# Kernel optimization log

Measured on AMD Instinct MI355X. Metric: run time of the kernel, lower is better.

Reference implementation:

```python
import jax, jax.numpy as jnp
import numpy as np

DEPTH = 3


def _gather_nei(feats, graph):
    # feats: [B, M, F], graph: [B, N, NB] -> [B, N, NB, F]
    return jax.vmap(lambda f, g: f[g])(feats, graph)


def setup_inputs() -> dict:
    B, N, NB, NBOND = 64, 120, 10, 250
    AF, BF, H = 82, 6, 300
    key = jax.random.key(0)
    ks = jax.random.split(key, 14)
    inp = {
        "atom_feats_1": jax.random.normal(ks[0], (B, N, AF), dtype=jnp.float32),
        "bond_feats": jax.random.normal(ks[1], (B, NBOND, BF), dtype=jnp.float32),
        "atom_graph": jax.random.randint(ks[2], (B, N, NB), 0, N, dtype=jnp.int64),
        "bond_graph": jax.random.randint(ks[3], (B, N, NB), 0, NBOND, dtype=jnp.int64),
        "num_nbs": jax.random.randint(ks[4], (B, N), 0, NB, dtype=jnp.int64),
        "n_atoms": jax.random.randint(ks[5], (B,), 1, N, dtype=jnp.int64),
        "mask_neis": jax.random.randint(ks[6], (B, N, NB, 1), 0, 2) > 0,
        "mask_atoms": jax.random.randint(ks[7], (B, N, 1), 0, 2) > 0,
        # parameters (Linear weights stored as [in, out]); dropout is eval-mode (identity)
        "W_fc1": jax.random.normal(ks[8], (AF, H), dtype=jnp.float32) * 0.05,
        "W_gc_nei": jax.random.normal(ks[9], (H + BF, H), dtype=jnp.float32) * 0.05,
        "b_gc_nei": jnp.zeros((H,), dtype=jnp.float32),
        "W_gc_atom": jax.random.normal(ks[10], (2 * H, H), dtype=jnp.float32) * 0.05,
        "b_gc_atom": jnp.zeros((H,), dtype=jnp.float32),
        "W_fc2a": jax.random.normal(ks[11], (H, H), dtype=jnp.float32) * 0.05,
        "W_fc2b": jax.random.normal(ks[12], (BF, H), dtype=jnp.float32) * 0.05,
        "W_fc2": jax.random.normal(ks[13], (H, H), dtype=jnp.float32) * 0.05,
    }
    return inp


def reference(atom_feats_1, bond_feats, atom_graph, bond_graph, num_nbs, n_atoms,
              mask_neis, mask_atoms, W_fc1, W_gc_nei, b_gc_nei, W_gc_atom,
              b_gc_atom, W_fc2a, W_fc2b, W_fc2):
    zero = jnp.float32(0)
    atom_feats = jax.nn.relu(atom_feats_1 @ W_fc1)                 # [B,N,H]
    bondnei_feats = _gather_nei(bond_feats, bond_graph)            # [B,N,NB,BF]
    local_feats = None
    for i in range(DEPTH):
        atomnei_feats = _gather_nei(atom_feats, atom_graph)        # [B,N,NB,H]
        if i + 1 == DEPTH:
            an = atomnei_feats @ W_fc2a                            # [B,N,NB,H]
            bn = bondnei_feats @ W_fc2b                            # [B,N,NB,H]
            nei = jnp.where(mask_neis, an * bn, zero).sum(-2)      # [B,N,H]
            self_feats = atom_feats @ W_fc2                        # [B,N,H]
            local_feats = jnp.where(mask_atoms, self_feats * nei, zero)
        else:
            cat = jnp.concatenate([atomnei_feats, bondnei_feats], axis=-1)
            nei = jax.nn.relu(cat @ W_gc_nei + b_gc_nei)           # [B,N,NB,H]
            nei = jnp.where(mask_neis, nei, zero).sum(-2)          # [B,N,H]
            update = jnp.concatenate([atom_feats, nei], axis=-1)   # [B,N,2H]
            atom_feats = jax.nn.relu(update @ W_gc_atom + b_gc_atom)
    return local_feats
```

## Files before the change

kernel.cpp:

```cpp
#include <hip/hip_runtime.h>
#include <hip/hip_bf16.h>

#define BATCH 64
#define NATOM 120
#define NNB 10
#define NBOND 250
#define AFDIM 82
#define BFDIM 6
#define HREAL 300
#define HP 320
#define NCT32 10
#define MA (BATCH*NATOM)
#define MB (BATCH*NBOND)

typedef short short8 __attribute__((ext_vector_type(8)));
typedef float f32x16 __attribute__((ext_vector_type(16)));
typedef unsigned int u32;
typedef u32 u32x2 __attribute__((ext_vector_type(2)));
typedef unsigned short u16;

__device__ __forceinline__ float bflo(u32 v) { return __builtin_bit_cast(float, v << 16); }
__device__ __forceinline__ float bfhi(u32 v) { return __builtin_bit_cast(float, v & 0xffff0000u); }
__device__ __forceinline__ u16 f2bf(float f) {
    __hip_bfloat16 h = __float2bfloat16(f);
    return __builtin_bit_cast(u16, h);
}

struct PackJob { const float* W; short8* dst; int Kreal, KT, KTfull, ktOff, blk0; };
struct Prep {
    const float* a1src; __hip_bfloat16* a1dst;
    const float* bsrc;  __hip_bfloat16* bdst;
    const int *mn, *agp, *bgp; u32* pk;
    PackJob j[8];
};

#define CONV1_BLKS 2880
#define CONV2_BLKS 2000
#define PACK_BASE  (CONV1_BLKS + CONV2_BLKS)
#define PACK_BLKS  275
#define PK_BASE    (PACK_BASE + PACK_BLKS)
#define PK_BLKS    300
#define PREP_BLKS  (PK_BASE + PK_BLKS)

__global__ __launch_bounds__(256) void prep_all(Prep cfg) {
    const int bid = blockIdx.x;
    const int tid = threadIdx.x;
    if (bid < CONV1_BLKS) {
        int id = bid * 256 + tid;
        int r = id / 96, c = id - r * 96;
        float f = (c < AFDIM) ? cfg.a1src[(size_t)r * AFDIM + c] : 0.f;
        cfg.a1dst[id] = __float2bfloat16(f);
    } else if (bid < PACK_BASE) {
        int id = (bid - CONV1_BLKS) * 256 + tid;
        int r = id >> 5, c = id & 31;
        float f = (c < BFDIM) ? cfg.bsrc[(size_t)r * BFDIM + c] : 0.f;
        cfg.bdst[id] = __float2bfloat16(f);
    } else if (bid < PK_BASE) {
        const int pid = bid - PACK_BASE;
        int ji = 0;
#pragma unroll
        for (int i = 1; i < 8; ++i) if (pid >= cfg.j[i].blk0) ji = i;
        const PackJob J = cfg.j[ji];
        int id = (pid - J.blk0) * 256 + tid;
        int n = NCT32 * J.KT * 64;
        if (id >= n) return;
        int lane = id & 63;
        int kt = (id >> 6) % J.KT;
        int ct = id / (J.KT * 64);
        int col = ct * 32 + (lane & 31);
        int kbase = kt * 16 + (lane >> 5) * 8;
        short8 v;
#pragma unroll
        for (int jj = 0; jj < 8; ++jj) {
            int k = kbase + jj;
            float f = (k < J.Kreal && col < HREAL) ? J.W[(size_t)k * HREAL + col] : 0.f;
            v[jj] = (short)f2bf(f);
        }
        J.dst[(size_t)(ct * J.KTfull + J.ktOff + kt) * 64 + lane] = v;
    } else {
        int id = (bid - PK_BASE) * 256 + tid;
        u32 w = 0;
        if (cfg.mn[id]) w = 0x80000000u | ((u32)cfg.agp[id] << 16) | (u32)cfg.bgp[id];
        cfg.pk[id] = w;
    }
}

template<int KT, int KT1, int WAVES, bool RELU, bool OUT1F, bool ADDF>
__device__ __forceinline__ void gemm_dev(
    int bx, int by, int tid,
    const __hip_bfloat16* __restrict__ A1,
    const __hip_bfloat16* __restrict__ A2,
    const short8* __restrict__ Wp,
    const float* __restrict__ bias0,
    const float* __restrict__ bias1,
    __hip_bfloat16* __restrict__ out0,
    __hip_bfloat16* __restrict__ out1,
    float* __restrict__ out1f,
    const float* __restrict__ addp) {
    const int lane = tid & 63;
    const int wv   = tid >> 6;
    const int m0   = bx * (32 * WAVES) + wv * 32;
    const int ct0  = by * 2;
    const int r1   = m0 + (lane & 31);
    const int koff = (lane >> 5) * 8;

    constexpr int S1  = KT1 * 16;
    constexpr int S2  = (KT - KT1) * 16;
    constexpr int CH  = (KT >= 10) ? 10 : KT;
    constexpr int NCH = KT / CH;

    f32x16 acc[2];
#pragma unroll
    for (int r = 0; r < 16; ++r) { acc[0][r] = 0.f; acc[1][r] = 0.f; }

    const short8* w0 = Wp + ((size_t)ct0 * KT) * 64 + lane;
    const short8* w1 = w0 + (size_t)KT * 64;

#pragma unroll
    for (int ch = 0; ch < NCH; ++ch) {
        short8 a[CH];
#pragma unroll
        for (int kt = 0; kt < CH; ++kt) {
            const int g = ch * CH + kt;
            if (g < KT1)
                a[kt] = *reinterpret_cast<const short8*>(A1 + (size_t)r1 * S1 + g * 16 + koff);
            else
                a[kt] = *reinterpret_cast<const short8*>(A2 + (size_t)r1 * S2 + (g - KT1) * 16 + koff);
        }
#pragma unroll
        for (int kt = 0; kt < CH; ++kt) {
            const int g = ch * CH + kt;
            acc[0] = __builtin_amdgcn_mfma_f32_32x32x16_bf16(a[kt], w0[(size_t)g * 64], acc[0], 0, 0, 0);
            acc[1] = __builtin_amdgcn_mfma_f32_32x32x16_bf16(a[kt], w1[(size_t)g * 64], acc[1], 0, 0, 0);
        }
    }

#pragma unroll
    for (int c = 0; c < 2; ++c) {
        const int ct = ct0 + c;
        const bool second = (ct >= NCT32);
        const int colb = second ? ct * 32 - HP : ct * 32;
        const int col = colb + (lane & 31);
        __hip_bfloat16* op = second ? out1 : out0;
        const float* bp = second ? bias1 : bias0;
        const float bb = (bp && col < HREAL) ? bp[col] : 0.f;
#pragma unroll
        for (int r = 0; r < 16; ++r) {
            const int row = m0 + (r & 3) + 8 * (r >> 2) + 4 * (lane >> 5);
            float v = acc[c][r] + bb;
            if (ADDF) v += addp[(size_t)row * HP + col];
            if (RELU) v = fmaxf(v, 0.f);
            if (second) {
                if (OUT1F) out1f[(size_t)row * HP + col] = v;
                else       out1[(size_t)row * HP + col] = __float2bfloat16(v);
            } else {
                op[(size_t)row * HP + col] = __float2bfloat16(v);
            }
        }
    }
}

#define FC1_BLKS  (MA/64 * 5)
#define BOND_BLKS (MB/64 * 10)
__global__ __launch_bounds__(128)
void k_input_gemms(const __hip_bfloat16* __restrict__ A1b,
                   const __hip_bfloat16* __restrict__ bondb,
                   const short8* __restrict__ pW1,
                   const short8* __restrict__ pWbd,
                   const float* __restrict__ bgn,
                   __hip_bfloat16* __restrict__ af0,
                   __hip_bfloat16* __restrict__ bondgc,
                   __hip_bfloat16* __restrict__ bnb) {
    const int bid = blockIdx.x;
    if (bid < FC1_BLKS) {
        gemm_dev<6, 6, 2, true, false, false>(bid % (MA/64), bid / (MA/64), threadIdx.x,
                                              A1b, A1b, pW1, nullptr, nullptr, af0, nullptr, nullptr, nullptr);
    } else {
        const int b2 = bid - FC1_BLKS;
        gemm_dev<2, 2, 2, false, false, false>(b2 % (MB/64), b2 / (MB/64), threadIdx.x,
                                               bondb, bondb, pWbd, bgn, nullptr, bondgc, bnb, nullptr, nullptr);
    }
}

__global__ __launch_bounds__(256)
void k_gemm_nu(const __hip_bfloat16* __restrict__ af, const short8* __restrict__ W,
               const float* __restrict__ bias1,
               __hip_bfloat16* __restrict__ Tb, float* __restrict__ U) {
    gemm_dev<20, 20, 4, false, true, false>(blockIdx.x, blockIdx.y, threadIdx.x,
                                            af, af, W, nullptr, bias1, Tb, nullptr, U, nullptr);
}

__global__ __launch_bounds__(128)
void k_gemm_bot(const __hip_bfloat16* __restrict__ neib, const short8* __restrict__ W,
                const float* __restrict__ U, __hip_bfloat16* __restrict__ afn) {
    gemm_dev<20, 20, 2, true, false, true>(blockIdx.x, blockIdx.y, threadIdx.x,
                                           neib, neib, W, nullptr, nullptr, afn, nullptr, nullptr, U);
}

__global__ __launch_bounds__(256)
void k_gemm_final(const __hip_bfloat16* __restrict__ af, const short8* __restrict__ W,
                  __hip_bfloat16* __restrict__ selfF, __hip_bfloat16* __restrict__ A2f) {
    gemm_dev<20, 20, 4, false, false, false>(blockIdx.x, blockIdx.y, threadIdx.x,
                                             af, af, W, nullptr, nullptr, selfF, A2f, nullptr, nullptr);
}

__global__ __launch_bounds__(320)
void gather2(const u32* __restrict__ T,
             const u32* __restrict__ BG,
             const u32* __restrict__ pk,
             u32* __restrict__ nei) {
    const int bn = blockIdx.x * 4 + threadIdx.x / 80;
    const int t2 = (threadIdx.x % 80) * 2;
    const int b  = bn / NATOM;
    const int base = bn * NNB;
    float lo0 = 0.f, hi0 = 0.f, lo1 = 0.f, hi1 = 0.f;
#pragma unroll
    for (int j = 0; j < NNB; ++j) {
        const u32 w = pk[base + j];
        if ((int)w < 0) {
            const int a  = (w >> 16) & 0xff;
            const int bo = w & 0xffff;
            u32x2 ta = *reinterpret_cast<const u32x2*>(T  + (size_t)(b * NATOM + a)  * 160 + t2);
            u32x2 tb = *reinterpret_cast<const u32x2*>(BG + (size_t)(b * NBOND + bo) * 160 + t2);
            lo0 += fmaxf(bflo(ta[0]) + bflo(tb[0]), 0.f);
            hi0 += fmaxf(bfhi(ta[0]) + bfhi(tb[0]), 0.f);
            lo1 += fmaxf(bflo(ta[1]) + bflo(tb[1]), 0.f);
            hi1 += fmaxf(bfhi(ta[1]) + bfhi(tb[1]), 0.f);
        }
    }
    u32x2 o;
    o[0] = (u32)f2bf(lo0) | ((u32)f2bf(hi0) << 16);
    o[1] = (u32)f2bf(lo1) | ((u32)f2bf(hi1) << 16);
    *reinterpret_cast<u32x2*>(nei + (size_t)bn * 160 + t2) = o;
}

__global__ __launch_bounds__(320)
void final2(const u32* __restrict__ A2f,
            const u32* __restrict__ bnb,
            const u32* __restrict__ selfF,
            const u32* __restrict__ pk,
            const int* __restrict__ maska,
            float* __restrict__ out) {
    const int bn = blockIdx.x * 4 + threadIdx.x / 80;
    const int tt = threadIdx.x % 80;
    if (tt >= 75) return;
    const int t2 = tt * 2;
    const int b  = bn / NATOM;
    const int base = bn * NNB;
    float lo0 = 0.f, hi0 = 0.f, lo1 = 0.f, hi1 = 0.f;
#pragma unroll
    for (int j = 0; j < NNB; ++j) {
        const u32 w = pk[base + j];
        if ((int)w < 0) {
            const int a  = (w >> 16) & 0xff;
            const int bo = w & 0xffff;
            u32x2 va = *reinterpret_cast<const u32x2*>(A2f + (size_t)(b * NATOM + a)  * 160 + t2);
            u32x2 vb = *reinterpret_cast<const u32x2*>(bnb + (size_t)(b * NBOND + bo) * 160 + t2);
            lo0 += bflo(va[0]) * bflo(vb[0]);
            hi0 += bfhi(va[0]) * bfhi(vb[0]);
            lo1 += bflo(va[1]) * bflo(vb[1]);
            hi1 += bfhi(va[1]) * bfhi(vb[1]);
        }
    }
    float4 r = make_float4(0.f, 0.f, 0.f, 0.f);
    if (maska[bn]) {
        u32x2 s = *reinterpret_cast<const u32x2*>(selfF + (size_t)bn * 160 + t2);
        r.x = bflo(s[0]) * lo0;
        r.y = bfhi(s[0]) * hi0;
        r.z = bflo(s[1]) * lo1;
        r.w = bfhi(s[1]) * hi1;
    }
    *reinterpret_cast<float4*>(out + (size_t)bn * HREAL + tt * 4) = r;
}

extern "C" void kernel_launch(void* const* d_in, const int* in_sizes, int n_in,
                              void* d_out, int out_size, void* d_ws, size_t ws_size,
                              hipStream_t stream) {
    const float* A1        = (const float*)d_in[0];
    const float* bond      = (const float*)d_in[1];
    const int*   ag        = (const int*)d_in[2];
    const int*   bg        = (const int*)d_in[3];
    const int*   maskn     = (const int*)d_in[6];
    const int*   maska     = (const int*)d_in[7];
    const float* W_fc1     = (const float*)d_in[8];
    const float* W_gc_nei  = (const float*)d_in[9];
    const float* b_gc_nei  = (const float*)d_in[10];
    const float* W_gc_atom = (const float*)d_in[11];
    const float* b_gc_atom = (const float*)d_in[12];
    const float* W_fc2a    = (const float*)d_in[13];
    const float* W_fc2b    = (const float*)d_in[14];
    const float* W_fc2     = (const float*)d_in[15];
    float* out = (float*)d_out;

    char* p = (char*)d_ws;
    auto alloc = [&](size_t bytes) { char* r = p; p += (bytes + 63) & ~(size_t)63; return r; };
    __hip_bfloat16* A1b    = (__hip_bfloat16*)alloc((size_t)MA * 96 * 2);
    __hip_bfloat16* bondb  = (__hip_bfloat16*)alloc((size_t)MB * 32 * 2);
    __hip_bfloat16* af0    = (__hip_bfloat16*)alloc((size_t)MA * HP * 2);
    __hip_bfloat16* af1    = (__hip_bfloat16*)alloc((size_t)MA * HP * 2);
    __hip_bfloat16* Tb     = (__hip_bfloat16*)alloc((size_t)MA * HP * 2);
    __hip_bfloat16* neib   = (__hip_bfloat16*)alloc((size_t)MA * HP * 2);
    __hip_bfloat16* selfF  = (__hip_bfloat16*)alloc((size_t)MA * HP * 2);
    __hip_bfloat16* A2f    = (__hip_bfloat16*)alloc((size_t)MA * HP * 2);
    __hip_bfloat16* bondgc = (__hip_bfloat16*)alloc((size_t)MB * HP * 2);
    __hip_bfloat16* bnb    = (__hip_bfloat16*)alloc((size_t)MB * HP * 2);
    float*          U      = (float*)alloc((size_t)MA * HP * 4);
    u32*            pk     = (u32*)alloc((size_t)MA * NNB * 4);
    short8* pW1  = (short8*)alloc((size_t)NCT32 * 6  * 64 * 16);
    short8* pWnei= (short8*)alloc((size_t)2 * NCT32 * 20 * 64 * 16);
    short8* pWgb = (short8*)alloc((size_t)NCT32 * 20 * 64 * 16);
    short8* pWbd = (short8*)alloc((size_t)2 * NCT32 * 2 * 64 * 16);
    short8* pWfd = (short8*)alloc((size_t)2 * NCT32 * 20 * 64 * 16);

    Prep cfg;
    cfg.a1src = A1;   cfg.a1dst = A1b;
    cfg.bsrc  = bond; cfg.bdst  = bondb;
    cfg.mn = maskn; cfg.agp = ag; cfg.bgp = bg; cfg.pk = pk;
    cfg.j[0] = { W_fc1,                             pW1,                         AFDIM, 6,  6,  0,   0 };
    cfg.j[1] = { W_gc_nei,                          pWnei,                       HREAL, 20, 20, 0,  15 };
    cfg.j[2] = { W_gc_atom,                         pWnei + (size_t)NCT32*20*64, HREAL, 20, 20, 0,  65 };
    cfg.j[3] = { W_gc_atom + (size_t)HREAL * HREAL, pWgb,                        HREAL, 20, 20, 0, 115 };
    cfg.j[4] = { W_gc_nei + (size_t)HREAL * HREAL,  pWbd,                        BFDIM, 2,  2,  0, 165 };
    cfg.j[5] = { W_fc2b,                            pWbd + (size_t)NCT32*2*64,   BFDIM, 2,  2,  0, 170 };
    cfg.j[6] = { W_fc2,                             pWfd,                        HREAL, 20, 20, 0, 175 };
    cfg.j[7] = { W_fc2a,                            pWfd + (size_t)NCT32*20*64,  HREAL, 20, 20, 0, 225 };
    prep_all<<<dim3(PREP_BLKS), dim3(256), 0, stream>>>(cfg);

    k_input_gemms<<<dim3(FC1_BLKS + BOND_BLKS), dim3(128), 0, stream>>>(
        A1b, bondb, pW1, pWbd, b_gc_nei, af0, bondgc, bnb);

    const dim3 gNU(MA / 128, 10);
    const dim3 gBOT(MA / 64, 5);
    const dim3 t256(256), t128(128);

    const __hip_bfloat16* af = af0;
    __hip_bfloat16* afn = af1;
    for (int it = 0; it < 2; ++it) {
        k_gemm_nu<<<gNU, t256, 0, stream>>>(af, pWnei, b_gc_atom, Tb, U);
        gather2<<<dim3(MA / 4), dim3(320), 0, stream>>>(
            (const u32*)Tb, (const u32*)bondgc, pk, (u32*)neib);
        k_gemm_bot<<<gBOT, t128, 0, stream>>>(neib, pWgb, U, afn);
        const __hip_bfloat16* t = afn; afn = (__hip_bfloat16*)af; af = t;
    }

    k_gemm_final<<<gNU, t256, 0, stream>>>(af, pWfd, selfF, A2f);
    final2<<<dim3(MA / 4), dim3(320), 0, stream>>>(
        (const u32*)A2f, (const u32*)bnb, (const u32*)selfF, pk, maska, out);
}
```

Baseline: 157.3 us.

## Stage per-molecule atom and bond tiles in LDS for neighbor gather kernels

Replaces the per-atom global-memory gather kernels with block-per-(molecule, 40-channel slice) kernels. Each block first copies the molecule's transformed atom rows, bond rows and packed neighbor list into shared memory, then does the neighbor sums from LDS. This targets repeated scattered global/L2 reads of neighbor rows. The cost is fewer blocks (512), about 34 KB of LDS per block, and a staging barrier. Some LDS bank conflicts are also possible from the random indices.

```diff
diff --git a/kernel.cpp b/kernel.cpp
--- a/kernel.cpp
+++ b/kernel.cpp
@@ -204,74 +204,119 @@
                                              af, af, W, nullptr, nullptr, selfF, A2f, nullptr, nullptr);
 }
 
-__global__ __launch_bounds__(320)
-void gather2(const u32* __restrict__ T,
-             const u32* __restrict__ BG,
-             const u32* __restrict__ pk,
-             u32* __restrict__ nei) {
-    const int bn = blockIdx.x * 4 + threadIdx.x / 80;
-    const int t2 = (threadIdx.x % 80) * 2;
-    const int b  = bn / NATOM;
-    const int base = bn * NNB;
-    float lo0 = 0.f, hi0 = 0.f, lo1 = 0.f, hi1 = 0.f;
-#pragma unroll
-    for (int j = 0; j < NNB; ++j) {
-        const u32 w = pk[base + j];
-        if ((int)w < 0) {
-            const int a  = (w >> 16) & 0xff;
-            const int bo = w & 0xffff;
-            u32x2 ta = *reinterpret_cast<const u32x2*>(T  + (size_t)(b * NATOM + a)  * 160 + t2);
-            u32x2 tb = *reinterpret_cast<const u32x2*>(BG + (size_t)(b * NBOND + bo) * 160 + t2);
-            lo0 += fmaxf(bflo(ta[0]) + bflo(tb[0]), 0.f);
-            hi0 += fmaxf(bfhi(ta[0]) + bfhi(tb[0]), 0.f);
-            lo1 += fmaxf(bflo(ta[1]) + bflo(tb[1]), 0.f);
-            hi1 += fmaxf(bfhi(ta[1]) + bfhi(tb[1]), 0.f);
-        }
-    }
-    u32x2 o;
-    o[0] = (u32)f2bf(lo0) | ((u32)f2bf(hi0) << 16);
-    o[1] = (u32)f2bf(lo1) | ((u32)f2bf(hi1) << 16);
-    *reinterpret_cast<u32x2*>(nei + (size_t)bn * 160 + t2) = o;
-}
-
-__global__ __launch_bounds__(320)
-void final2(const u32* __restrict__ A2f,
-            const u32* __restrict__ bnb,
-            const u32* __restrict__ selfF,
-            const u32* __restrict__ pk,
-            const int* __restrict__ maska,
-            float* __restrict__ out) {
-    const int bn = blockIdx.x * 4 + threadIdx.x / 80;
-    const int tt = threadIdx.x % 80;
-    if (tt >= 75) return;
-    const int t2 = tt * 2;
-    const int b  = bn / NATOM;
-    const int base = bn * NNB;
-    float lo0 = 0.f, hi0 = 0.f, lo1 = 0.f, hi1 = 0.f;
-#pragma unroll
-    for (int j = 0; j < NNB; ++j) {
-        const u32 w = pk[base + j];
-        if ((int)w < 0) {
-            const int a  = (w >> 16) & 0xff;
-            const int bo = w & 0xffff;
-            u32x2 va = *reinterpret_cast<const u32x2*>(A2f + (size_t)(b * NATOM + a)  * 160 + t2);
-            u32x2 vb = *reinterpret_cast<const u32x2*>(bnb + (size_t)(b * NBOND + bo) * 160 + t2);
-            lo0 += bflo(va[0]) * bflo(vb[0]);
-            hi0 += bfhi(va[0]) * bfhi(vb[0]);
-            lo1 += bflo(va[1]) * bflo(vb[1]);
-            hi1 += bfhi(va[1]) * bfhi(vb[1]);
-        }
-    }
-    float4 r = make_float4(0.f, 0.f, 0.f, 0.f);
-    if (maska[bn]) {
-        u32x2 s = *reinterpret_cast<const u32x2*>(selfF + (size_t)bn * 160 + t2);
-        r.x = bflo(s[0]) * lo0;
-        r.y = bfhi(s[0]) * hi0;
-        r.z = bflo(s[1]) * lo1;
-        r.w = bfhi(s[1]) * hi1;
-    }
-    *reinterpret_cast<float4*>(out + (size_t)bn * HREAL + tt * 4) = r;
-}
+#define GBLK (BATCH * 8)
+__global__ __launch_bounds__(512)
+void gather_lds(const u32* __restrict__ T,
+                const u32* __restrict__ BG,
+                const u32* __restrict__ pk,
+                u32* __restrict__ nei) {
+    extern __shared__ u32 sm[];
+    u32* TL = sm;
+    u32* BL = sm + 120 * 20;
+    u32* PL = BL + 250 * 20;
+    const int b   = blockIdx.x >> 3;
+    const int c0  = (blockIdx.x & 7) * 20;
+    const int tid = threadIdx.x;
+
+    for (int i = tid; i < 120 * 10; i += 512) {
+        int r = i / 10, p = i - r * 10;
+        *reinterpret_cast<u32x2*>(&TL[r * 20 + 2 * p]) =
+            *reinterpret_cast<const u32x2*>(T + (size_t)(b * NATOM + r) * (HP / 2) + c0 + 2 * p);
+    }
+    for (int i = tid; i < 250 * 10; i += 512) {
+        int r = i / 10, p = i - r * 10;
+        *reinterpret_cast<u32x2*>(&BL[r * 20 + 2 * p]) =
+            *reinterpret_cast<const u32x2*>(BG + (size_t)(b * NBOND + r) * (HP / 2) + c0 + 2 * p);
+    }
+    for (int i = tid; i < NATOM * NNB; i += 512) PL[i] = pk[b * NATOM * NNB + i];
+    __syncthreads();
+
+    for (int i = tid; i < 120 * 10; i += 512) {
+        const int row = i / 10, p = i - row * 10;
+        float lo0 = 0.f, hi0 = 0.f, lo1 = 0.f, hi1 = 0.f;
+#pragma unroll
+        for (int j = 0; j < NNB; ++j) {
+            const u32 w = PL[row * NNB + j];
+            if ((int)w < 0) {
+                const int a  = (w >> 16) & 0xff;
+                const int bo = w & 0xffff;
+                u32x2 ta = *reinterpret_cast<const u32x2*>(&TL[a * 20 + 2 * p]);
+                u32x2 tb = *reinterpret_cast<const u32x2*>(&BL[bo * 20 + 2 * p]);
+                lo0 += fmaxf(bflo(ta[0]) + bflo(tb[0]), 0.f);
+                hi0 += fmaxf(bfhi(ta[0]) + bfhi(tb[0]), 0.f);
+                lo1 += fmaxf(bflo(ta[1]) + bflo(tb[1]), 0.f);
+                hi1 += fmaxf(bfhi(ta[1]) + bfhi(tb[1]), 0.f);
+            }
+        }
+        u32x2 o;
+        o[0] = (u32)f2bf(lo0) | ((u32)f2bf(hi0) << 16);
+        o[1] = (u32)f2bf(lo1) | ((u32)f2bf(hi1) << 16);
+        *reinterpret_cast<u32x2*>(nei + (size_t)(b * NATOM + row) * (HP / 2) + c0 + 2 * p) = o;
+    }
+}
+#define GATHER_LDS_BYTES ((120*20 + 250*20 + 1200) * 4)
+
+__global__ __launch_bounds__(512)
+void final_lds(const u32* __restrict__ A2f,
+               const u32* __restrict__ bnb,
+               const u32* __restrict__ selfF,
+               const u32* __restrict__ pk,
+               const int* __restrict__ maska,
+               float* __restrict__ out) {
+    extern __shared__ u32 sm[];
+    u32* AL = sm;
+    u32* BL = sm + 120 * 20;
+    u32* PL = BL + 250 * 20;
+    u32* ML = PL + 1200;
+    const int b   = blockIdx.x >> 3;
+    const int c0  = (blockIdx.x & 7) * 20;
+    const int tid = threadIdx.x;
+
+    for (int i = tid; i < 120 * 10; i += 512) {
+        int r = i / 10, p = i - r * 10;
+        *reinterpret_cast<u32x2*>(&AL[r * 20 + 2 * p]) =
+            *reinterpret_cast<const u32x2*>(A2f + (size_t)(b * NATOM + r) * (HP / 2) + c0 + 2 * p);
+    }
+    for (int i = tid; i < 250 * 10; i += 512) {
+        int r = i / 10, p = i - r * 10;
+        *reinterpret_cast<u32x2*>(&BL[r * 20 + 2 * p]) =
+            *reinterpret_cast<const u32x2*>(bnb + (size_t)(b * NBOND + r) * (HP / 2) + c0 + 2 * p);
+    }
+    for (int i = tid; i < NATOM * NNB; i += 512) PL[i] = pk[b * NATOM * NNB + i];
+    for (int i = tid; i < NATOM; i += 512) ML[i] = (u32)(maska[b * NATOM + i] != 0);
+    __syncthreads();
+
+    for (int i = tid; i < 120 * 10; i += 512) {
+        const int row = i / 10, p = i - row * 10;
+        const int cA = c0 + 2 * p;
+        if (cA >= 150) continue;
+        float lo0 = 0.f, hi0 = 0.f, lo1 = 0.f, hi1 = 0.f;
+#pragma unroll
+        for (int j = 0; j < NNB; ++j) {
+            const u32 w = PL[row * NNB + j];
+            if ((int)w < 0) {
+                const int a  = (w >> 16) & 0xff;
+                const int bo = w & 0xffff;
+                u32x2 va = *reinterpret_cast<const u32x2*>(&AL[a * 20 + 2 * p]);
+                u32x2 vb = *reinterpret_cast<const u32x2*>(&BL[bo * 20 + 2 * p]);
+                lo0 += bflo(va[0]) * bflo(vb[0]);
+                hi0 += bfhi(va[0]) * bfhi(vb[0]);
+                lo1 += bflo(va[1]) * bflo(vb[1]);
+                hi1 += bfhi(va[1]) * bfhi(vb[1]);
+            }
+        }
+        float4 r4 = make_float4(0.f, 0.f, 0.f, 0.f);
+        if (ML[row]) {
+            u32x2 s = *reinterpret_cast<const u32x2*>(selfF + (size_t)(b * NATOM + row) * (HP / 2) + cA);
+            r4.x = bflo(s[0]) * lo0;
+            r4.y = bfhi(s[0]) * hi0;
+            r4.z = bflo(s[1]) * lo1;
+            r4.w = bfhi(s[1]) * hi1;
+        }
+        *reinterpret_cast<float4*>(out + (size_t)(b * NATOM + row) * HREAL + 2 * cA) = r4;
+    }
+}
+#define FINAL_LDS_BYTES ((120*20 + 250*20 + 1200 + 120) * 4)
 
 extern "C" void kernel_launch(void* const* d_in, const int* in_sizes, int n_in,
                               void* d_out, int out_size, void* d_ws, size_t ws_size,
@@ -331,19 +376,19 @@
 
     const dim3 gNU(MA / 128, 10);
     const dim3 gBOT(MA / 64, 5);
-    const dim3 t256(256), t128(128);
+    const dim3 t256(256), t128(128), t512(512);
 
     const __hip_bfloat16* af = af0;
     __hip_bfloat16* afn = af1;
     for (int it = 0; it < 2; ++it) {
         k_gemm_nu<<<gNU, t256, 0, stream>>>(af, pWnei, b_gc_atom, Tb, U);
-        gather2<<<dim3(MA / 4), dim3(320), 0, stream>>>(
+        gather_lds<<<dim3(GBLK), t512, GATHER_LDS_BYTES, stream>>>(
             (const u32*)Tb, (const u32*)bondgc, pk, (u32*)neib);
         k_gemm_bot<<<gBOT, t128, 0, stream>>>(neib, pWgb, U, afn);
         const __hip_bfloat16* t = afn; afn = (__hip_bfloat16*)af; af = t;
     }
 
     k_gemm_final<<<gNU, t256, 0, stream>>>(af, pWfd, selfF, A2f);
-    final2<<<dim3(MA / 4), dim3(320), 0, stream>>>(
+    final_lds<<<dim3(GBLK), t512, FINAL_LDS_BYTES, stream>>>(
         (const u32*)A2f, (const u32*)bnb, (const u32*)selfF, pk, maska, out);
 }
```

After: 142.8 us. 9.2% less time.
